# Optimization experiments

Measured on AMD Instinct MI355X. Metric: run time of the kernel, lower is better.

## Reference

```python
import jax, jax.numpy as jnp
import numpy as np

B, S, DIM = 1, 1024, 512
H, DH = 8, 64
CB = 32   # compress block size
SB = 32   # selection block size (== CB, so no importance remap)
NSEL, NMEM, WIN = 4, 4, 64
SCALE = DH ** -0.5
EPS = 1.1920929e-07  # torch fp32 finfo eps used by nn.RMSNorm


def _rmsnorm(x, g):
    return x * jax.lax.rsqrt(jnp.mean(x * x, -1, keepdims=True) + EPS) * g


def _rope(t):
    # lucidrains rotary: interleaved pairs, theta=10000, positions 0..n-1
    d = t.shape[-1]
    inv = 1.0 / (10000.0 ** (jnp.arange(0, d, 2, dtype=jnp.float32) / d))
    ang = jnp.arange(t.shape[-2], dtype=jnp.float32)[:, None] * inv   # [n, d/2]
    cos = jnp.repeat(jnp.cos(ang), 2, axis=-1)
    sin = jnp.repeat(jnp.sin(ang), 2, axis=-1)
    tp = t.reshape(t.shape[:-1] + (d // 2, 2))
    rot = jnp.stack((-tp[..., 1], tp[..., 0]), -1).reshape(t.shape)
    return t * cos + rot * sin


def setup_inputs():
    key = jax.random.key(0)
    ks = jax.random.split(key, 12)
    cd = CB * DH
    p = lambda k, shp: jax.random.normal(k, shp, jnp.float32) * 0.02
    return {
        'inp': jax.random.normal(ks[0], (B, S, DIM), jnp.float32),
        'norm_g': jnp.ones((DIM,), jnp.float32),
        'w_qkv': p(ks[1], (DIM, 3 * H * DH)),
        'k_pos': p(ks[2], (H, CB, DH)),
        'v_pos': p(ks[3], (H, CB, DH)),
        'kc_w1': p(ks[4], (cd, cd)), 'kc_b1': jnp.zeros((cd,), jnp.float32),
        'kc_w2': p(ks[5], (cd, DH)), 'kc_b2': jnp.zeros((DH,), jnp.float32),
        'vc_w1': p(ks[6], (cd, cd)), 'vc_b1': jnp.zeros((cd,), jnp.float32),
        'vc_w2': p(ks[7], (cd, DH)), 'vc_b2': jnp.zeros((DH,), jnp.float32),
        'mem_kv': p(ks[8], (2, H, NMEM, DH)),
        'strat_w': p(ks[9], (DIM, 3 * H)),
        'strat_b': jnp.tile(jnp.array([-2.0, -2.0, 2.0], jnp.float32), H),
        'out_w': p(ks[10], (H * DH, DIM)),
    }


def reference(inp, norm_g, w_qkv, k_pos, v_pos, kc_w1, kc_b1, kc_w2, kc_b2,
              vc_w1, vc_b1, vc_w2, vc_b2, mem_kv, strat_w, strat_b, out_w):
    NEG = -jnp.finfo(inp.dtype).max
    x = _rmsnorm(inp, norm_g)
    q, k, v = jnp.split(x @ w_qkv, 3, axis=-1)
    sh = lambda t: t.reshape(B, S, H, DH).transpose(0, 2, 1, 3)   # b h n d
    q, k, v = sh(q), sh(k), sh(v)

    # ---- compressed branch ----
    nb = S // CB
    kb = k.reshape(B, H, nb, CB, DH) + k_pos[None, :, None]
    vb = v.reshape(B, H, nb, CB, DH) + v_pos[None, :, None]
    comp = lambda t, w1, b1, w2, b2: jax.nn.relu(
        t.reshape(B, H, nb, CB * DH) @ w1 + b1) @ w2 + b2
    ck = comp(kb, kc_w1, kc_b1, kc_w2, kc_b2)                     # b h nb d
    cv = comp(vb, vc_w1, vc_b1, vc_w2, vc_b2)
    ck = jnp.concatenate([jnp.broadcast_to(mem_kv[0][None], (B, H, NMEM, DH)), ck], 2)
    cv = jnp.concatenate([jnp.broadcast_to(mem_kv[1][None], (B, H, NMEM, DH)), cv], 2)

    csim = jnp.einsum('bhid,bhjd->bhij', q, ck) * SCALE
    pos = jnp.arange(S)
    ckpos = jnp.concatenate([jnp.full((NMEM,), -1), (jnp.arange(nb) + 1) * CB - 1])
    csim = jnp.where(ckpos[None, :] < pos[:, None], csim, NEG)
    cattn = jax.nn.softmax(csim, -1)
    c_out = jnp.einsum('bhij,bhjd->bhid', cattn, cv)

    rq, rk = _rope(q), _rope(k)

    # ---- fine selected branch (CB == SB => importance maps 1:1) ----
    imp = cattn[..., NMEM:]                                       # b h i nb
    sel_vals, sel_idx = jax.lax.top_k(imp, NSEL)                  # b h i k
    own = pos // SB
    sel_idx = jnp.concatenate(
        [sel_idx, jnp.broadcast_to(own[None, None, :, None], (B, H, S, 1))], -1)
    fmask = jnp.broadcast_to((sel_vals > 1e-10)[..., None], (B, H, S, NSEL, SB))
    causal = jnp.tril(jnp.ones((SB, SB), bool))[pos % SB]         # [S, SB]
    fmask = jnp.concatenate(
        [fmask, jnp.broadcast_to(causal[None, None, :, None, :], (B, H, S, 1, SB))], 3)
    fmask = fmask.reshape(B, H, S, (NSEL + 1) * SB)

    fkb = rk.reshape(B, H, nb, SB, DH)
    fvb = v.reshape(B, H, nb, SB, DH)
    gather = jax.vmap(jax.vmap(lambda blk, idx: blk[idx]))        # per (b,h)
    fk = gather(fkb, sel_idx).reshape(B, H, S, (NSEL + 1) * SB, DH)
    fv = gather(fvb, sel_idx).reshape(B, H, S, (NSEL + 1) * SB, DH)
    fsim = jnp.einsum('bhid,bhijd->bhij', rq, fk) * SCALE
    fattn = jax.nn.softmax(jnp.where(fmask, fsim, NEG), -1)
    f_out = jnp.einsum('bhij,bhijd->bhid', fattn, fv)

    # ---- sliding window branch (LocalAttention, causal, exact window) ----
    ssim = jnp.einsum('bhid,bhjd->bhij', rq, rk) * SCALE
    smask = (pos[None, :] <= pos[:, None]) & (pos[:, None] - pos[None, :] <= WIN)
    sattn = jax.nn.softmax(jnp.where(smask, ssim, NEG), -1)
    s_out = jnp.einsum('bhij,bhjd->bhid', sattn, v)

    # ---- gated combine ----
    strat = jax.nn.sigmoid(x @ strat_w + strat_b)
    strat = strat.reshape(B, S, H, 3).transpose(0, 2, 1, 3)       # b h n s
    out = strat[..., 0:1] * c_out + strat[..., 1:2] * f_out + strat[..., 2:3] * s_out
    return out.transpose(0, 2, 1, 3).reshape(B, S, H * DH) @ out_w
```

## Files before the change

### kernel.cpp

```cpp
#include <hip/hip_runtime.h>
#include <hip/hip_bf16.h>
#include <cfloat>
#include <math.h>

#define S_LEN 1024
#define DIM 512
#define H_N 8
#define DH 64
#define CB 32
#define NB 32
#define NSEL 4
#define NMEM 4
#define WIN 64
#define SCALE 0.125f
#define EPS 1.1920929e-07f

#define OFF_X      0u
#define OFF_QKV    524288u
#define OFF_RQ     2097152u
#define OFF_RK     2621440u
#define OFF_COS    3145728u
#define OFF_SIN    3178496u
#define OFF_TK     3211264u
#define OFF_TV     3735552u
#define OFF_HK     4259840u
#define OFF_HV     4784128u
#define OFF_CKC    5308416u
#define OFF_CVC    5324800u
#define OFF_STRAT  5341184u
#define OFF_ATT    5365760u
#define OFF_QKVP   2097152u
#define OFF_COMPP  5890048u
#define OFF_OUTP   5890048u

__global__ void rmsnorm_strat_k(const float* __restrict__ inp, const float* __restrict__ g,
                                const float* __restrict__ sw, const float* __restrict__ sb,
                                float* __restrict__ x, float* __restrict__ strat) {
    int s = blockIdx.x;
    int t = threadIdx.x;
    __shared__ __align__(16) float xs[512];
    __shared__ float red[24][8];
    float v0 = inp[s * DIM + t];
    float v1 = inp[s * DIM + t + 256];
    float ss = v0 * v0 + v1 * v1;
    for (int o = 32; o > 0; o >>= 1) ss += __shfl_xor(ss, o);
    __shared__ float wsum[4];
    int wid = t >> 6, lane = t & 63;
    if (lane == 0) wsum[wid] = ss;
    __syncthreads();
    float tot = wsum[0] + wsum[1] + wsum[2] + wsum[3];
    float scale = 1.0f / sqrtf(tot / (float)DIM + EPS);
    float x0 = v0 * scale * g[t];
    float x1 = v1 * scale * g[t + 256];
    x[s * DIM + t]       = x0;
    x[s * DIM + t + 256] = x1;
    xs[t] = x0;
    xs[t + 256] = x1;
    __syncthreads();
    if (t < 192) {
        int o = t >> 3, p = t & 7;
        float acc = 0.0f;
        const float* xb = xs + p * 64;
        for (int k = 0; k < 64; ++k) acc += xb[k] * sw[(p * 64 + k) * 24 + o];
        red[o][p] = acc;
    }
    __syncthreads();
    if (t < 24) {
        float a = sb[t];
        for (int p = 0; p < 8; ++p) a += red[t][p];
        strat[s * 24 + t] = 1.0f / (1.0f + expf(-a));
    }
}

__global__ void rope_table_k(float* __restrict__ cost, float* __restrict__ sint) {
    int idx = blockIdx.x * 256 + threadIdx.x;
    int s = idx >> 5, i = idx & 31;
    double inv = pow(10000.0, -(double)(2 * i) / 64.0);
    double ang = (double)s * inv;
    cost[idx] = (float)cos(ang);
    sint[idx] = (float)sin(ang);
}

__global__ void rope_apply_k(const float* __restrict__ qkv, const float* __restrict__ cost,
                             const float* __restrict__ sint,
                             float* __restrict__ rq, float* __restrict__ rk) {
    int idx = blockIdx.x * 256 + threadIdx.x;
    int s = idx >> 8;
    int rem = idx & 255;
    int h = rem >> 5, i = rem & 31;
    float c = cost[s * 32 + i], sn = sint[s * 32 + i];
    int qb = s * 1536 + h * 64 + 2 * i;
    float q0 = qkv[qb], q1 = qkv[qb + 1];
    int ob = s * 512 + h * 64 + 2 * i;
    rq[ob]     = q0 * c - q1 * sn;
    rq[ob + 1] = q1 * c + q0 * sn;
    float k0 = qkv[qb + 512], k1 = qkv[qb + 513];
    rk[ob]     = k0 * c - k1 * sn;
    rk[ob + 1] = k1 * c + k0 * sn;
}

__global__ void tkv_k(const float* __restrict__ qkv, const float* __restrict__ k_pos,
                      const float* __restrict__ v_pos,
                      float* __restrict__ tk, float* __restrict__ tv) {
    int idx = blockIdx.x * 256 + threadIdx.x;
    int row = idx >> 11;
    int c = idx & 2047;
    int h = row >> 5, nb = row & 31;
    int cb = c >> 6, d = c & 63;
    int srow = nb * 32 + cb;
    tk[idx] = qkv[srow * 1536 + 512 + h * 64 + d] + k_pos[(h * 32 + cb) * 64 + d];
    tv[idx] = qkv[srow * 1536 + 1024 + h * 64 + d] + v_pos[(h * 32 + cb) * 64 + d];
}

__device__ __forceinline__ void gemm_sk_body(const float* __restrict__ A, const float* __restrict__ B,
                                             float* __restrict__ P, int M, int N, int K,
                                             int kstart, int Ks) {
    __shared__ __align__(16) float As[2][16][68];
    __shared__ __align__(16) float Bs[2][16][64];
    const int bm = blockIdx.x * 64, bn = blockIdx.y * 64;
    const int tid = threadIdx.x;
    const int tx = tid & 15, ty = tid >> 4;
    const int ar = tid >> 2;
    const int ac = (tid & 3) * 4;
    const int br = tid >> 4;
    const int bc = (tid & 15) * 4;
    const float* Aptr = A + (size_t)(bm + ar) * K + kstart + ac;
    const float* Bptr = B + (size_t)(kstart + br) * N + bn + bc;

    float4 a4 = *(const float4*)(Aptr);
    float4 b4 = *(const float4*)(Bptr);
    float acc[4][4] = {};
    int buf = 0;
    for (int k0 = 0; k0 < Ks; k0 += 16) {
        As[buf][ac + 0][ar] = a4.x;
        As[buf][ac + 1][ar] = a4.y;
        As[buf][ac + 2][ar] = a4.z;
        As[buf][ac + 3][ar] = a4.w;
        *(float4*)&Bs[buf][br][bc] = b4;
        __syncthreads();
        if (k0 + 16 < Ks) {
            a4 = *(const float4*)(Aptr + k0 + 16);
            b4 = *(const float4*)(Bptr + (size_t)(k0 + 16) * N);
        }
#pragma unroll
        for (int kk = 0; kk < 16; ++kk) {
            const float4 af = *(const float4*)&As[buf][kk][ty * 4];
            const float4 bf = *(const float4*)&Bs[buf][kk][tx * 4];
            acc[0][0] += af.x * bf.x; acc[0][1] += af.x * bf.y; acc[0][2] += af.x * bf.z; acc[0][3] += af.x * bf.w;
            acc[1][0] += af.y * bf.x; acc[1][1] += af.y * bf.y; acc[1][2] += af.y * bf.z; acc[1][3] += af.y * bf.w;
            acc[2][0] += af.z * bf.x; acc[2][1] += af.z * bf.y; acc[2][2] += af.z * bf.z; acc[2][3] += af.z * bf.w;
            acc[3][0] += af.w * bf.x; acc[3][1] += af.w * bf.y; acc[3][2] += af.w * bf.z; acc[3][3] += af.w * bf.w;
        }
        buf ^= 1;
    }
#pragma unroll
    for (int i = 0; i < 4; ++i) {
        int m = bm + ty * 4 + i;
        float4 v;
        v.x = acc[i][0]; v.y = acc[i][1]; v.z = acc[i][2]; v.w = acc[i][3];
        *(float4*)&P[(size_t)m * N + bn + tx * 4] = v;
    }
}

__global__ void gemm_sk_k(const float* __restrict__ A, const float* __restrict__ B,
                          float* __restrict__ P, int M, int N, int K, int nsplit) {
    int kz = blockIdx.z;
    int Ks = K / nsplit;
    gemm_sk_body(A, B, P + (size_t)kz * M * N, M, N, K, kz * Ks, Ks);
}

__global__ void gemm_comp_k(const float* __restrict__ A0, const float* __restrict__ B0,
                            const float* __restrict__ A1, const float* __restrict__ B1,
                            float* __restrict__ P, int M, int N, int K) {
    int z = blockIdx.z;
    int g = z >> 2, kz = z & 3;
    const float* A = g ? A1 : A0;
    const float* B = g ? B1 : B0;
    int Ks = K >> 2;
    gemm_sk_body(A, B, P + (size_t)z * M * N, M, N, K, kz * Ks, Ks);
}

template <int NS, bool RELU, bool BIAS>
__global__ void reduce_k(const float* __restrict__ P, const float* __restrict__ bias,
                         float* __restrict__ Y, int MN, int N) {
    int idx4 = blockIdx.x * 256 + threadIdx.x;
    if (idx4 * 4 >= MN) return;
    const float4* p4 = (const float4*)P;
    int mn4 = MN >> 2;
    float4 v = p4[idx4];
#pragma unroll
    for (int j = 1; j < NS; ++j) {
        float4 w = p4[idx4 + j * (size_t)mn4];
        v.x += w.x; v.y += w.y; v.z += w.z; v.w += w.w;
    }
    if (BIAS) {
        int col = (idx4 * 4) % N;
        float4 b = *(const float4*)(bias + col);
        v.x += b.x; v.y += b.y; v.z += b.z; v.w += b.w;
    }
    if (RELU) {
        v.x = fmaxf(v.x, 0.f); v.y = fmaxf(v.y, 0.f);
        v.z = fmaxf(v.z, 0.f); v.w = fmaxf(v.w, 0.f);
    }
    ((float4*)Y)[idx4] = v;
}

__device__ __forceinline__ void skinny_body(const float* __restrict__ A, const float* __restrict__ B,
                                            const float* __restrict__ bias, float* __restrict__ C, int K) {
    int row = blockIdx.x;
    int col = threadIdx.x & 63;
    int chunk = threadIdx.x >> 6;
    int kpc = K >> 2;
    const float* a = A + (size_t)row * K + chunk * kpc;
    const float* b = B + (size_t)chunk * kpc * 64;
    float acc = 0.0f;
    for (int k = 0; k < kpc; k += 4) {
        float4 av = *(const float4*)(a + k);
        acc += av.x * b[(k + 0) * 64 + col];
        acc += av.y * b[(k + 1) * 64 + col];
        acc += av.z * b[(k + 2) * 64 + col];
        acc += av.w * b[(k + 3) * 64 + col];
    }
    __shared__ float red[4][64];
    red[chunk][col] = acc;
    __syncthreads();
    if (chunk == 0)
        C[(size_t)row * 64 + col] = red[0][col] + red[1][col] + red[2][col] + red[3][col] + bias[col];
}

__global__ void gemm_skinny_z2_k(const float* __restrict__ A0, const float* __restrict__ B0,
                                 const float* __restrict__ b0, float* __restrict__ C0,
                                 const float* __restrict__ A1, const float* __restrict__ B1,
                                 const float* __restrict__ b1, float* __restrict__ C1, int K) {
    if (blockIdx.z == 0) skinny_body(A0, B0, b0, C0, K);
    else                 skinny_body(A1, B1, b1, C1, K);
}

__device__ __forceinline__ float dot64(const float* __restrict__ qsh, const float* __restrict__ kr) {
    const float4* q4 = (const float4*)qsh;
    const float4* k4 = (const float4*)kr;
    float acc = 0.0f;
#pragma unroll
    for (int i = 0; i < 16; ++i) {
        float4 q = q4[i], k = k4[i];
        acc += q.x * k.x + q.y * k.y + q.z * k.z + q.w * k.w;
    }
    return acc;
}

__device__ __forceinline__ float redmax64(float v) {
    for (int o = 32; o > 0; o >>= 1) v = fmaxf(v, __shfl_xor(v, o));
    return v;
}
__device__ __forceinline__ float redsum64(float v) {
    for (int o = 32; o > 0; o >>= 1) v += __shfl_xor(v, o);
    return v;
}

__global__ void attn_fused_k(const float* __restrict__ qkv, const float* __restrict__ rq,
                             const float* __restrict__ rk, const float* __restrict__ ckc,
                             const float* __restrict__ cvc, const float* __restrict__ mem_kv,
                             const float* __restrict__ strat, float* __restrict__ att) {
    int s = blockIdx.x, h = blockIdx.y, lane = threadIdx.x;
    __shared__ __align__(16) float qs[64];
    __shared__ __align__(16) float rqs[64];
    __shared__ float pa[192];
    __shared__ int rows[192];
    qs[lane]  = qkv[s * 1536 + h * 64 + lane];
    rqs[lane] = rq[s * 512 + h * 64 + lane];
    __syncthreads();

    float sim = -FLT_MAX;
    if (lane < 36) {
        bool valid = (lane < NMEM) || ((lane - NMEM + 1) * CB - 1 < s);
        if (valid) {
            const float* kr = (lane < NMEM) ? (mem_kv + (h * 4 + lane) * 64)
                                            : (ckc + (h * 32 + lane - NMEM) * 64);
            sim = dot64(qs, kr) * SCALE;
        }
    }
    float mx = redmax64(sim);
    float e = (sim == -FLT_MAX) ? 0.0f : expf(sim - mx);
    float tot = redsum64(e);
    float a = e / tot;
    pa[lane] = (lane < 36) ? a : 0.0f;
    __syncthreads();
    float c_acc = 0.0f;
    for (int j = 0; j < NMEM; ++j)
        c_acc += pa[j] * mem_kv[2048 + (h * 4 + j) * 64 + lane];
    for (int j = 0; j < 32; ++j)
        c_acc += pa[NMEM + j] * cvc[(h * 32 + j) * 64 + lane];

    float tval = (lane >= NMEM && lane < 36) ? a : -1.0f;
    int tidx = lane - NMEM;
    int sel0, sel1, sel2, sel3, msk = 0;
#pragma unroll
    for (int t = 0; t < NSEL; ++t) {
        float bv = tval; int bi = tidx;
        for (int o = 32; o > 0; o >>= 1) {
            float ov = __shfl_xor(bv, o);
            int oi = __shfl_xor(bi, o);
            if (ov > bv || (ov == bv && oi < bi)) { bv = ov; bi = oi; }
        }
        if (t == 0) sel0 = bi; else if (t == 1) sel1 = bi;
        else if (t == 2) sel2 = bi; else sel3 = bi;
        if (bv > 1e-10f) msk |= 1 << t;
        if (tidx == bi && lane >= NMEM && lane < 36) tval = -1.0f;
    }

    int own = s >> 5, p = s & 31, t31 = lane & 31;
    bool hi = lane >= 32;
    int blkA = hi ? sel1 : sel0;
    bool valA = hi ? (msk & 2) : (msk & 1);
    int rowA = blkA * 32 + t31;
    float simA = valA ? dot64(rqs, rk + rowA * 512 + h * 64) * SCALE : -FLT_MAX;
    int blkB = hi ? sel3 : sel2;
    bool valB = hi ? (msk & 8) : (msk & 4);
    int rowB = blkB * 32 + t31;
    float simB = valB ? dot64(rqs, rk + rowB * 512 + h * 64) * SCALE : -FLT_MAX;
    int rowC = own * 32 + t31;
    bool valC = (!hi) && (t31 <= p);
    float simC = valC ? dot64(rqs, rk + rowC * 512 + h * 64) * SCALE : -FLT_MAX;

    float fmx = redmax64(fmaxf(fmaxf(simA, simB), simC));
    float eA = (simA == -FLT_MAX) ? 0.0f : expf(simA - fmx);
    float eB = (simB == -FLT_MAX) ? 0.0f : expf(simB - fmx);
    float eC = (simC == -FLT_MAX) ? 0.0f : expf(simC - fmx);
    float fsum = redsum64(eA + eB + eC);
    float finv = 1.0f / fsum;
    pa[lane] = eA * finv;        rows[lane] = rowA;
    pa[64 + lane] = eB * finv;   rows[64 + lane] = rowB;
    pa[128 + lane] = eC * finv;  rows[128 + lane] = rowC;
    __syncthreads();
    float f_acc = 0.0f;
    for (int kk = 0; kk < 160; ++kk)
        f_acc += pa[kk] * qkv[rows[kk] * 1536 + 1024 + h * 64 + lane];
    __syncthreads();

    int lo = (s > WIN) ? s - WIN : 0;
    int cnt = s - lo + 1;
    float sA = (lane < cnt) ? dot64(rqs, rk + (lo + lane) * 512 + h * 64) * SCALE : -FLT_MAX;
    float sB = (64 + lane < cnt) ? dot64(rqs, rk + (lo + 64 + lane) * 512 + h * 64) * SCALE : -FLT_MAX;
    float smx = redmax64(fmaxf(sA, sB));
    float esA = (sA == -FLT_MAX) ? 0.0f : expf(sA - smx);
    float esB = (sB == -FLT_MAX) ? 0.0f : expf(sB - smx);
    float ssum = redsum64(esA + esB);
    float sinv = 1.0f / ssum;
    pa[lane] = esA * sinv;
    if (64 + lane < cnt) pa[64 + lane] = esB * sinv;
    __syncthreads();
    float s_acc = 0.0f;
    for (int kk = 0; kk < cnt; ++kk)
        s_acc += pa[kk] * qkv[(lo + kk) * 1536 + 1024 + h * 64 + lane];

    const float* st = strat + s * 24 + h * 3;
    att[s * 512 + h * 64 + lane] = st[0] * c_acc + st[1] * f_acc + st[2] * s_acc;
}

extern "C" void kernel_launch(void* const* d_in, const int* in_sizes, int n_in,
                              void* d_out, int out_size, void* d_ws, size_t ws_size,
                              hipStream_t stream) {
    const float* inp     = (const float*)d_in[0];
    const float* norm_g  = (const float*)d_in[1];
    const float* w_qkv   = (const float*)d_in[2];
    const float* k_pos   = (const float*)d_in[3];
    const float* v_pos   = (const float*)d_in[4];
    const float* kc_w1   = (const float*)d_in[5];
    const float* kc_b1   = (const float*)d_in[6];
    const float* kc_w2   = (const float*)d_in[7];
    const float* kc_b2   = (const float*)d_in[8];
    const float* vc_w1   = (const float*)d_in[9];
    const float* vc_b1   = (const float*)d_in[10];
    const float* vc_w2   = (const float*)d_in[11];
    const float* vc_b2   = (const float*)d_in[12];
    const float* mem_kv  = (const float*)d_in[13];
    const float* strat_w = (const float*)d_in[14];
    const float* strat_b = (const float*)d_in[15];
    const float* out_w   = (const float*)d_in[16];
    float* out = (float*)d_out;

    float* ws = (float*)d_ws;
    float* x     = ws + OFF_X;
    float* qkv   = ws + OFF_QKV;
    float* rq    = ws + OFF_RQ;
    float* rk    = ws + OFF_RK;
    float* cost  = ws + OFF_COS;
    float* sint  = ws + OFF_SIN;
    float* tk    = ws + OFF_TK;
    float* tv    = ws + OFF_TV;
    float* hk    = ws + OFF_HK;
    float* hv    = ws + OFF_HV;
    float* ckc   = ws + OFF_CKC;
    float* cvc   = ws + OFF_CVC;
    float* strat = ws + OFF_STRAT;
    float* att   = ws + OFF_ATT;
    float* qkvp  = ws + OFF_QKVP;
    float* compp = ws + OFF_COMPP;
    float* outp  = ws + OFF_OUTP;

    rmsnorm_strat_k<<<1024, 256, 0, stream>>>(inp, norm_g, strat_w, strat_b, x, strat);
    gemm_sk_k<<<dim3(16, 24, 2), 256, 0, stream>>>(x, w_qkv, qkvp, 1024, 1536, 512, 2);
    reduce_k<2, false, false><<<1536, 256, 0, stream>>>(qkvp, nullptr, qkv, 1024 * 1536, 1536);
    rope_table_k<<<128, 256, 0, stream>>>(cost, sint);
    rope_apply_k<<<1024, 256, 0, stream>>>(qkv, cost, sint, rq, rk);
    tkv_k<<<2048, 256, 0, stream>>>(qkv, k_pos, v_pos, tk, tv);
    gemm_comp_k<<<dim3(4, 32, 8), 256, 0, stream>>>(tk, kc_w1, tv, vc_w1, compp, 256, 2048, 2048);
    reduce_k<4, true, true><<<512, 256, 0, stream>>>(compp, kc_b1, hk, 256 * 2048, 2048);
    reduce_k<4, true, true><<<512, 256, 0, stream>>>(compp + 4u * 256 * 2048, vc_b1, hv, 256 * 2048, 2048);
    gemm_skinny_z2_k<<<dim3(256, 1, 2), 256, 0, stream>>>(hk, kc_w2, kc_b2, ckc, hv, vc_w2, vc_b2, cvc, 2048);
    attn_fused_k<<<dim3(1024, 8), 64, 0, stream>>>(qkv, rq, rk, ckc, cvc, mem_kv, strat, att);
    gemm_sk_k<<<dim3(16, 8, 4), 256, 0, stream>>>(att, out_w, outp, 1024, 512, 512, 4);
    reduce_k<4, false, false><<<512, 256, 0, stream>>>(outp, nullptr, out, 1024 * 512, 512);
}
```

Measured before the change: 375.4 us.

## Transpose K/V layouts for coalesced attention and fuse prep kernels into GEMM loads

Adds transposed per-head rk and compressed-key buffers so each lane in the attention kernel reads keys with coalesced, d-major loads instead of strided 64-float dot products per lane. V is also copied into a per-head contiguous buffer during the QKV reduction. The tkv add-position step is folded into the compression GEMM's A loads, the rope table kernel is folded into rope_apply, and the two compression reductions are merged into one launch. Zero-weight rows are skipped in the selection gather. The cost is an extra transpose kernel and a rearranged workspace, and the transposed key reads are scattered gathers when the selected rows differ across lanes.

```diff
diff --git a/kernel.cpp b/kernel.cpp
--- a/kernel.cpp
+++ b/kernel.cpp
@@ -16,22 +16,19 @@
 #define EPS 1.1920929e-07f
 
 #define OFF_X      0u
+#define OFF_RKT    0u
 #define OFF_QKV    524288u
 #define OFF_RQ     2097152u
 #define OFF_RK     2621440u
-#define OFF_COS    3145728u
-#define OFF_SIN    3178496u
-#define OFF_TK     3211264u
-#define OFF_TV     3735552u
-#define OFF_HK     4259840u
-#define OFF_HV     4784128u
-#define OFF_CKC    5308416u
-#define OFF_CVC    5324800u
-#define OFF_STRAT  5341184u
-#define OFF_ATT    5365760u
-#define OFF_QKVP   2097152u
-#define OFF_COMPP  5890048u
-#define OFF_OUTP   5890048u
+#define OFF_VBUF   3145728u
+#define OFF_CKT    3670016u
+#define OFF_CVC    3702784u
+#define OFF_STRAT  3735552u
+#define OFF_ATT    3760128u
+#define OFF_HK     4284416u
+#define OFF_QKVP   5332992u
+#define OFF_COMPP  5332992u
+#define OFF_OUTP   5332992u
 
 __global__ void rmsnorm_strat_k(const float* __restrict__ inp, const float* __restrict__ g,
                                 const float* __restrict__ sw, const float* __restrict__ sb,
@@ -70,46 +67,6 @@
         for (int p = 0; p < 8; ++p) a += red[t][p];
         strat[s * 24 + t] = 1.0f / (1.0f + expf(-a));
     }
-}
-
-__global__ void rope_table_k(float* __restrict__ cost, float* __restrict__ sint) {
-    int idx = blockIdx.x * 256 + threadIdx.x;
-    int s = idx >> 5, i = idx & 31;
-    double inv = pow(10000.0, -(double)(2 * i) / 64.0);
-    double ang = (double)s * inv;
-    cost[idx] = (float)cos(ang);
-    sint[idx] = (float)sin(ang);
-}
-
-__global__ void rope_apply_k(const float* __restrict__ qkv, const float* __restrict__ cost,
-                             const float* __restrict__ sint,
-                             float* __restrict__ rq, float* __restrict__ rk) {
-    int idx = blockIdx.x * 256 + threadIdx.x;
-    int s = idx >> 8;
-    int rem = idx & 255;
-    int h = rem >> 5, i = rem & 31;
-    float c = cost[s * 32 + i], sn = sint[s * 32 + i];
-    int qb = s * 1536 + h * 64 + 2 * i;
-    float q0 = qkv[qb], q1 = qkv[qb + 1];
-    int ob = s * 512 + h * 64 + 2 * i;
-    rq[ob]     = q0 * c - q1 * sn;
-    rq[ob + 1] = q1 * c + q0 * sn;
-    float k0 = qkv[qb + 512], k1 = qkv[qb + 513];
-    rk[ob]     = k0 * c - k1 * sn;
-    rk[ob + 1] = k1 * c + k0 * sn;
-}
-
-__global__ void tkv_k(const float* __restrict__ qkv, const float* __restrict__ k_pos,
-                      const float* __restrict__ v_pos,
-                      float* __restrict__ tk, float* __restrict__ tv) {
-    int idx = blockIdx.x * 256 + threadIdx.x;
-    int row = idx >> 11;
-    int c = idx & 2047;
-    int h = row >> 5, nb = row & 31;
-    int cb = c >> 6, d = c & 63;
-    int srow = nb * 32 + cb;
-    tk[idx] = qkv[srow * 1536 + 512 + h * 64 + d] + k_pos[(h * 32 + cb) * 64 + d];
-    tv[idx] = qkv[srow * 1536 + 1024 + h * 64 + d] + v_pos[(h * 32 + cb) * 64 + d];
 }
 
 __device__ __forceinline__ void gemm_sk_body(const float* __restrict__ A, const float* __restrict__ B,
@@ -169,20 +126,155 @@
     gemm_sk_body(A, B, P + (size_t)kz * M * N, M, N, K, kz * Ks, Ks);
 }
 
-__global__ void gemm_comp_k(const float* __restrict__ A0, const float* __restrict__ B0,
-                            const float* __restrict__ A1, const float* __restrict__ B1,
-                            float* __restrict__ P, int M, int N, int K) {
-    int z = blockIdx.z;
-    int g = z >> 2, kz = z & 3;
-    const float* A = g ? A1 : A0;
-    const float* B = g ? B1 : B0;
-    int Ks = K >> 2;
-    gemm_sk_body(A, B, P + (size_t)z * M * N, M, N, K, kz * Ks, Ks);
-}
-
-template <int NS, bool RELU, bool BIAS>
-__global__ void reduce_k(const float* __restrict__ P, const float* __restrict__ bias,
-                         float* __restrict__ Y, int MN, int N) {
+__global__ void reduce_qkv_k(const float* __restrict__ P, float* __restrict__ qkv,
+                             float* __restrict__ vbuf) {
+    int idx4 = blockIdx.x * 256 + threadIdx.x;
+    const int mn4 = 393216;
+    float4 v = ((const float4*)P)[idx4];
+    float4 w = ((const float4*)P)[idx4 + mn4];
+    v.x += w.x; v.y += w.y; v.z += w.z; v.w += w.w;
+    ((float4*)qkv)[idx4] = v;
+    int c = (idx4 % 384) * 4;
+    if (c >= 1024) {
+        int s = idx4 / 384;
+        int h = (c - 1024) >> 6, d = (c - 1024) & 63;
+        *(float4*)(vbuf + (size_t)h * 65536 + s * 64 + d) = v;
+    }
+}
+
+__global__ void rope_apply_k(const float* __restrict__ qkv,
+                             float* __restrict__ rq, float* __restrict__ rk) {
+    int idx = blockIdx.x * 256 + threadIdx.x;
+    int s = idx >> 8;
+    int rem = idx & 255;
+    int h = rem >> 5, i = rem & 31;
+    double inv = pow(10000.0, -(double)i / 32.0);
+    double ang = (double)s * inv;
+    float c = (float)cos(ang), sn = (float)sin(ang);
+    int qb = s * 1536 + h * 64 + 2 * i;
+    float q0 = qkv[qb], q1 = qkv[qb + 1];
+    int ob = s * 512 + h * 64 + 2 * i;
+    rq[ob]     = q0 * c - q1 * sn;
+    rq[ob + 1] = q1 * c + q0 * sn;
+    float k0 = qkv[qb + 512], k1 = qkv[qb + 513];
+    rk[ob]     = k0 * c - k1 * sn;
+    rk[ob + 1] = k1 * c + k0 * sn;
+}
+
+__global__ void transpose_rk_k(const float* __restrict__ rk, float* __restrict__ rkT,
+                               const float* __restrict__ mem_kv, float* __restrict__ ckT) {
+    int h = blockIdx.x, st = blockIdx.y, t = threadIdx.x;
+    __shared__ float tile[64][65];
+    int s0 = st * 64;
+    int r = t >> 2, c0 = (t & 3) * 16;
+    const float* src = rk + (size_t)(s0 + r) * 512 + h * 64 + c0;
+#pragma unroll
+    for (int q = 0; q < 4; ++q) {
+        float4 v = *(const float4*)(src + q * 4);
+        tile[r][c0 + q * 4 + 0] = v.x;
+        tile[r][c0 + q * 4 + 1] = v.y;
+        tile[r][c0 + q * 4 + 2] = v.z;
+        tile[r][c0 + q * 4 + 3] = v.w;
+    }
+    __syncthreads();
+    int wv = t >> 6, ls = t & 63;
+    float* dst = rkT + (size_t)h * 65536 + s0 + ls;
+#pragma unroll
+    for (int p = 0; p < 16; ++p) {
+        int d = p * 4 + wv;
+        dst[(size_t)d * 1024] = tile[ls][d];
+    }
+    if (st == 0) {
+        int d = t >> 2, j = t & 3;
+        ckT[h * 2304 + d * 36 + j] = mem_kv[h * 256 + j * 64 + d];
+    }
+}
+
+__global__ void gemm_comp_k(const float* __restrict__ qkv, const float* __restrict__ k_pos,
+                            const float* __restrict__ v_pos, const float* __restrict__ kw1,
+                            const float* __restrict__ vw1, float* __restrict__ P) {
+    int z = blockIdx.z, g = z >> 2, kz = z & 3;
+    const float* B = g ? vw1 : kw1;
+    const float* pos = g ? v_pos : k_pos;
+    const int qoff = g ? 1024 : 512;
+    const int kstart = kz * 512;
+    __shared__ __align__(16) float As[2][16][68];
+    __shared__ __align__(16) float Bs[2][16][64];
+    const int bm = blockIdx.x * 64, bn = blockIdx.y * 64;
+    const int tid = threadIdx.x;
+    const int tx = tid & 15, ty = tid >> 4;
+    const int ar = tid >> 2, ac = (tid & 3) * 4;
+    const int br = tid >> 4, bc = (tid & 15) * 4;
+    const int m = bm + ar;
+    const int hh = m >> 5, nb = m & 31;
+    const float* qb = qkv + (size_t)(nb * 32) * 1536 + qoff + hh * 64;
+    const float* pb = pos + hh * 2048;
+    const float* Bptr = B + (size_t)(kstart + br) * 2048 + bn + bc;
+
+    auto loadA = [&](int kk) {
+        int cb = kk >> 6, d = kk & 63;
+        float4 a = *(const float4*)(qb + (size_t)cb * 1536 + d);
+        float4 p = *(const float4*)(pb + cb * 64 + d);
+        a.x += p.x; a.y += p.y; a.z += p.z; a.w += p.w;
+        return a;
+    };
+
+    float4 a4 = loadA(kstart + ac);
+    float4 b4 = *(const float4*)Bptr;
+    float acc[4][4] = {};
+    int buf = 0;
+    for (int k0 = 0; k0 < 512; k0 += 16) {
+        As[buf][ac + 0][ar] = a4.x;
+        As[buf][ac + 1][ar] = a4.y;
+        As[buf][ac + 2][ar] = a4.z;
+        As[buf][ac + 3][ar] = a4.w;
+        *(float4*)&Bs[buf][br][bc] = b4;
+        __syncthreads();
+        if (k0 + 16 < 512) {
+            a4 = loadA(kstart + ac + k0 + 16);
+            b4 = *(const float4*)(Bptr + (size_t)(k0 + 16) * 2048);
+        }
+#pragma unroll
+        for (int kk = 0; kk < 16; ++kk) {
+            const float4 af = *(const float4*)&As[buf][kk][ty * 4];
+            const float4 bf = *(const float4*)&Bs[buf][kk][tx * 4];
+            acc[0][0] += af.x * bf.x; acc[0][1] += af.x * bf.y; acc[0][2] += af.x * bf.z; acc[0][3] += af.x * bf.w;
+            acc[1][0] += af.y * bf.x; acc[1][1] += af.y * bf.y; acc[1][2] += af.y * bf.z; acc[1][3] += af.y * bf.w;
+            acc[2][0] += af.z * bf.x; acc[2][1] += af.z * bf.y; acc[2][2] += af.z * bf.z; acc[2][3] += af.z * bf.w;
+            acc[3][0] += af.w * bf.x; acc[3][1] += af.w * bf.y; acc[3][2] += af.w * bf.z; acc[3][3] += af.w * bf.w;
+        }
+        buf ^= 1;
+    }
+    float* Pz = P + (size_t)z * 524288;
+#pragma unroll
+    for (int i = 0; i < 4; ++i) {
+        int mm = bm + ty * 4 + i;
+        float4 v;
+        v.x = acc[i][0]; v.y = acc[i][1]; v.z = acc[i][2]; v.w = acc[i][3];
+        *(float4*)&Pz[(size_t)mm * 2048 + bn + tx * 4] = v;
+    }
+}
+
+__global__ void reduce_comp_k(const float* __restrict__ P, const float* __restrict__ kb,
+                              const float* __restrict__ vb, float* __restrict__ hkv) {
+    int idx4 = blockIdx.x * 256 + threadIdx.x;
+    const int half4 = 131072;
+    int which = idx4 >= half4 ? 1 : 0;
+    int l4 = idx4 - which * half4;
+    const float4* p4 = (const float4*)P + (size_t)which * 4 * half4 + l4;
+    float4 v = p4[0];
+    float4 w1 = p4[half4], w2 = p4[2 * half4], w3 = p4[3 * (size_t)half4];
+    v.x += w1.x + w2.x + w3.x; v.y += w1.y + w2.y + w3.y;
+    v.z += w1.z + w2.z + w3.z; v.w += w1.w + w2.w + w3.w;
+    int col = (l4 * 4) & 2047;
+    const float* bias = (which ? vb : kb) + col;
+    v.x = fmaxf(v.x + bias[0], 0.f); v.y = fmaxf(v.y + bias[1], 0.f);
+    v.z = fmaxf(v.z + bias[2], 0.f); v.w = fmaxf(v.w + bias[3], 0.f);
+    *(float4*)(hkv + (size_t)which * 524288 + (size_t)l4 * 4) = v;
+}
+
+template <int NS>
+__global__ void reduce_k(const float* __restrict__ P, float* __restrict__ Y, int MN) {
     int idx4 = blockIdx.x * 256 + threadIdx.x;
     if (idx4 * 4 >= MN) return;
     const float4* p4 = (const float4*)P;
@@ -190,31 +282,27 @@
     float4 v = p4[idx4];
 #pragma unroll
     for (int j = 1; j < NS; ++j) {
-        float4 w = p4[idx4 + j * (size_t)mn4];
+        float4 w = p4[idx4 + (size_t)j * mn4];
         v.x += w.x; v.y += w.y; v.z += w.z; v.w += w.w;
     }
-    if (BIAS) {
-        int col = (idx4 * 4) % N;
-        float4 b = *(const float4*)(bias + col);
-        v.x += b.x; v.y += b.y; v.z += b.z; v.w += b.w;
-    }
-    if (RELU) {
-        v.x = fmaxf(v.x, 0.f); v.y = fmaxf(v.y, 0.f);
-        v.z = fmaxf(v.z, 0.f); v.w = fmaxf(v.w, 0.f);
-    }
     ((float4*)Y)[idx4] = v;
 }
 
-__device__ __forceinline__ void skinny_body(const float* __restrict__ A, const float* __restrict__ B,
-                                            const float* __restrict__ bias, float* __restrict__ C, int K) {
+__global__ void gemm_skinny_z2_k(const float* __restrict__ hkv, const float* __restrict__ kw2,
+                                 const float* __restrict__ kb2, const float* __restrict__ vw2,
+                                 const float* __restrict__ vb2, float* __restrict__ ckT,
+                                 float* __restrict__ cvc) {
+    int z = blockIdx.z;
+    const float* A = hkv + (size_t)z * 524288;
+    const float* B = z ? vw2 : kw2;
+    const float* bias = z ? vb2 : kb2;
     int row = blockIdx.x;
     int col = threadIdx.x & 63;
     int chunk = threadIdx.x >> 6;
-    int kpc = K >> 2;
-    const float* a = A + (size_t)row * K + chunk * kpc;
-    const float* b = B + (size_t)chunk * kpc * 64;
+    const float* a = A + (size_t)row * 2048 + chunk * 512;
+    const float* b = B + (size_t)chunk * 512 * 64;
     float acc = 0.0f;
-    for (int k = 0; k < kpc; k += 4) {
+    for (int k = 0; k < 512; k += 4) {
         float4 av = *(const float4*)(a + k);
         acc += av.x * b[(k + 0) * 64 + col];
         acc += av.y * b[(k + 1) * 64 + col];
@@ -224,28 +312,12 @@
     __shared__ float red[4][64];
     red[chunk][col] = acc;
     __syncthreads();
-    if (chunk == 0)
-        C[(size_t)row * 64 + col] = red[0][col] + red[1][col] + red[2][col] + red[3][col] + bias[col];
-}
-
-__global__ void gemm_skinny_z2_k(const float* __restrict__ A0, const float* __restrict__ B0,
-                                 const float* __restrict__ b0, float* __restrict__ C0,
-                                 const float* __restrict__ A1, const float* __restrict__ B1,
-                                 const float* __restrict__ b1, float* __restrict__ C1, int K) {
-    if (blockIdx.z == 0) skinny_body(A0, B0, b0, C0, K);
-    else                 skinny_body(A1, B1, b1, C1, K);
-}
-
-__device__ __forceinline__ float dot64(const float* __restrict__ qsh, const float* __restrict__ kr) {
-    const float4* q4 = (const float4*)qsh;
-    const float4* k4 = (const float4*)kr;
-    float acc = 0.0f;
-#pragma unroll
-    for (int i = 0; i < 16; ++i) {
-        float4 q = q4[i], k = k4[i];
-        acc += q.x * k.x + q.y * k.y + q.z * k.z + q.w * k.w;
-    }
-    return acc;
+    if (chunk == 0) {
+        float v = red[0][col] + red[1][col] + red[2][col] + red[3][col] + bias[col];
+        int hh = row >> 5, j = row & 31;
+        if (z == 0) ckT[hh * 2304 + col * 36 + 4 + j] = v;
+        else        cvc[(size_t)row * 64 + col] = v;
+    }
 }
 
 __device__ __forceinline__ float redmax64(float v) {
@@ -257,39 +329,61 @@
     return v;
 }
 
-__global__ void attn_fused_k(const float* __restrict__ qkv, const float* __restrict__ rq,
-                             const float* __restrict__ rk, const float* __restrict__ ckc,
-                             const float* __restrict__ cvc, const float* __restrict__ mem_kv,
-                             const float* __restrict__ strat, float* __restrict__ att) {
+__global__ __launch_bounds__(64) void attn_fused_k(
+    const float* __restrict__ qkv, const float* __restrict__ rq,
+    const float* __restrict__ rkT, const float* __restrict__ ckT,
+    const float* __restrict__ cvc, const float* __restrict__ mem_kv,
+    const float* __restrict__ vbuf, const float* __restrict__ strat,
+    float* __restrict__ att) {
     int s = blockIdx.x, h = blockIdx.y, lane = threadIdx.x;
     __shared__ __align__(16) float qs[64];
     __shared__ __align__(16) float rqs[64];
-    __shared__ float pa[192];
-    __shared__ int rows[192];
+    __shared__ float paw[192];
+    __shared__ int rww[192];
     qs[lane]  = qkv[s * 1536 + h * 64 + lane];
     rqs[lane] = rq[s * 512 + h * 64 + lane];
     __syncthreads();
 
-    float sim = -FLT_MAX;
-    if (lane < 36) {
-        bool valid = (lane < NMEM) || ((lane - NMEM + 1) * CB - 1 < s);
-        if (valid) {
-            const float* kr = (lane < NMEM) ? (mem_kv + (h * 4 + lane) * 64)
-                                            : (ckc + (h * 32 + lane - NMEM) * 64);
-            sim = dot64(qs, kr) * SCALE;
-        }
-    }
-    float mx = redmax64(sim);
-    float e = (sim == -FLT_MAX) ? 0.0f : expf(sim - mx);
+    int own = s >> 5, p = s & 31, t31 = lane & 31;
+    bool hiw = lane >= 32;
+    int lo = (s > WIN) ? s - WIN : 0;
+    int cnt = s - lo + 1;
+    bool cvalid = (lane < NMEM) || (lane < 36 && (lane - NMEM + 1) * CB - 1 < s);
+    int jc = (lane < 36) ? lane : 35;
+    int rowC = own * 32 + t31;
+    int rowSA = lo + lane;      if (rowSA > 1023) rowSA = 1023;
+    int rowSB = lo + 64 + lane; if (rowSB > 1023) rowSB = 1023;
+    const float* rkTh = rkT + (size_t)h * 65536;
+    const float* ckTh = ckT + h * 2304;
+
+    float c0 = 0, c1 = 0, f0 = 0, f1 = 0, a0 = 0, a1 = 0, b0 = 0, b1 = 0;
+#pragma unroll 4
+    for (int d = 0; d < 64; d += 2) {
+        float qd0 = qs[d], qd1 = qs[d + 1];
+        float rd0 = rqs[d], rd1 = rqs[d + 1];
+        const float* r0 = rkTh + (size_t)d * 1024;
+        const float* r1 = r0 + 1024;
+        c0 += qd0 * ckTh[d * 36 + jc];
+        c1 += qd1 * ckTh[(d + 1) * 36 + jc];
+        f0 += rd0 * r0[rowC];  f1 += rd1 * r1[rowC];
+        a0 += rd0 * r0[rowSA]; a1 += rd1 * r1[rowSA];
+        b0 += rd0 * r0[rowSB]; b1 += rd1 * r1[rowSB];
+    }
+
+    float simc = cvalid ? (c0 + c1) * SCALE : -FLT_MAX;
+    float mx = redmax64(simc);
+    float e = (simc == -FLT_MAX) ? 0.0f : expf(simc - mx);
     float tot = redsum64(e);
     float a = e / tot;
-    pa[lane] = (lane < 36) ? a : 0.0f;
-    __syncthreads();
-    float c_acc = 0.0f;
-    for (int j = 0; j < NMEM; ++j)
-        c_acc += pa[j] * mem_kv[2048 + (h * 4 + j) * 64 + lane];
-    for (int j = 0; j < 32; ++j)
-        c_acc += pa[NMEM + j] * cvc[(h * 32 + j) * 64 + lane];
+    paw[lane] = (lane < 36) ? a : 0.0f;
+    __syncthreads();
+    float cacc;
+    {
+        const float* mv = mem_kv + 2048 + h * 256 + lane;
+        cacc = paw[0] * mv[0] + paw[1] * mv[64] + paw[2] * mv[128] + paw[3] * mv[192];
+        const float* cvb = cvc + h * 2048 + lane;
+        for (int j = 0; j < 32; ++j) cacc += paw[4 + j] * cvb[j * 64];
+    }
 
     float tval = (lane >= NMEM && lane < 36) ? a : -1.0f;
     int tidx = lane - NMEM;
@@ -308,19 +402,23 @@
         if (tidx == bi && lane >= NMEM && lane < 36) tval = -1.0f;
     }
 
-    int own = s >> 5, p = s & 31, t31 = lane & 31;
-    bool hi = lane >= 32;
-    int blkA = hi ? sel1 : sel0;
-    bool valA = hi ? (msk & 2) : (msk & 1);
-    int rowA = blkA * 32 + t31;
-    float simA = valA ? dot64(rqs, rk + rowA * 512 + h * 64) * SCALE : -FLT_MAX;
-    int blkB = hi ? sel3 : sel2;
-    bool valB = hi ? (msk & 8) : (msk & 4);
-    int rowB = blkB * 32 + t31;
-    float simB = valB ? dot64(rqs, rk + rowB * 512 + h * 64) * SCALE : -FLT_MAX;
-    int rowC = own * 32 + t31;
-    bool valC = (!hi) && (t31 <= p);
-    float simC = valC ? dot64(rqs, rk + rowC * 512 + h * 64) * SCALE : -FLT_MAX;
+    int rowA = (hiw ? sel1 : sel0) * 32 + t31;
+    int rowB = (hiw ? sel3 : sel2) * 32 + t31;
+    float A0 = 0, A1 = 0, B0 = 0, B1 = 0;
+#pragma unroll 4
+    for (int d = 0; d < 64; d += 2) {
+        float rd0 = rqs[d], rd1 = rqs[d + 1];
+        const float* r0 = rkTh + (size_t)d * 1024;
+        const float* r1 = r0 + 1024;
+        A0 += rd0 * r0[rowA]; A1 += rd1 * r1[rowA];
+        B0 += rd0 * r0[rowB]; B1 += rd1 * r1[rowB];
+    }
+    bool valA = hiw ? ((msk >> 1) & 1) : (msk & 1);
+    bool valB = hiw ? ((msk >> 3) & 1) : ((msk >> 2) & 1);
+    bool valC = (!hiw) && (t31 <= p);
+    float simA = valA ? (A0 + A1) * SCALE : -FLT_MAX;
+    float simB = valB ? (B0 + B1) * SCALE : -FLT_MAX;
+    float simC = valC ? (f0 + f1) * SCALE : -FLT_MAX;
 
     float fmx = redmax64(fmaxf(fmaxf(simA, simB), simC));
     float eA = (simA == -FLT_MAX) ? 0.0f : expf(simA - fmx);
@@ -328,33 +426,36 @@
     float eC = (simC == -FLT_MAX) ? 0.0f : expf(simC - fmx);
     float fsum = redsum64(eA + eB + eC);
     float finv = 1.0f / fsum;
-    pa[lane] = eA * finv;        rows[lane] = rowA;
-    pa[64 + lane] = eB * finv;   rows[64 + lane] = rowB;
-    pa[128 + lane] = eC * finv;  rows[128 + lane] = rowC;
-    __syncthreads();
-    float f_acc = 0.0f;
-    for (int kk = 0; kk < 160; ++kk)
-        f_acc += pa[kk] * qkv[rows[kk] * 1536 + 1024 + h * 64 + lane];
-    __syncthreads();
-
-    int lo = (s > WIN) ? s - WIN : 0;
-    int cnt = s - lo + 1;
-    float sA = (lane < cnt) ? dot64(rqs, rk + (lo + lane) * 512 + h * 64) * SCALE : -FLT_MAX;
-    float sB = (64 + lane < cnt) ? dot64(rqs, rk + (lo + 64 + lane) * 512 + h * 64) * SCALE : -FLT_MAX;
+    __syncthreads();
+    paw[lane] = eA * finv;        rww[lane] = rowA;
+    paw[64 + lane] = eB * finv;   rww[64 + lane] = rowB;
+    paw[128 + lane] = eC * finv;  rww[128 + lane] = rowC;
+    __syncthreads();
+    const float* vh = vbuf + (size_t)h * 65536 + lane;
+    float facc = 0.0f;
+    for (int kk = 0; kk < 160; ++kk) {
+        float w = paw[kk];
+        if (w != 0.0f) facc += w * vh[(size_t)rww[kk] * 64];
+    }
+    __syncthreads();
+
+    float sA = (lane < cnt) ? (a0 + a1) * SCALE : -FLT_MAX;
+    float sB = (64 + lane < cnt) ? (b0 + b1) * SCALE : -FLT_MAX;
     float smx = redmax64(fmaxf(sA, sB));
     float esA = (sA == -FLT_MAX) ? 0.0f : expf(sA - smx);
     float esB = (sB == -FLT_MAX) ? 0.0f : expf(sB - smx);
     float ssum = redsum64(esA + esB);
     float sinv = 1.0f / ssum;
-    pa[lane] = esA * sinv;
-    if (64 + lane < cnt) pa[64 + lane] = esB * sinv;
-    __syncthreads();
-    float s_acc = 0.0f;
+    paw[lane] = esA * sinv;
+    if (64 + lane < cnt) paw[64 + lane] = esB * sinv;
+    __syncthreads();
+    float sacc = 0.0f;
+    const float* vlo = vh + (size_t)lo * 64;
     for (int kk = 0; kk < cnt; ++kk)
-        s_acc += pa[kk] * qkv[(lo + kk) * 1536 + 1024 + h * 64 + lane];
+        sacc += paw[kk] * vlo[(size_t)kk * 64];
 
     const float* st = strat + s * 24 + h * 3;
-    att[s * 512 + h * 64 + lane] = st[0] * c_acc + st[1] * f_acc + st[2] * s_acc;
+    att[s * 512 + h * 64 + lane] = st[0] * cacc + st[1] * facc + st[2] * sacc;
 }
 
 extern "C" void kernel_launch(void* const* d_in, const int* in_sizes, int n_in,
@@ -381,34 +482,29 @@
 
     float* ws = (float*)d_ws;
     float* x     = ws + OFF_X;
+    float* rkT   = ws + OFF_RKT;
     float* qkv   = ws + OFF_QKV;
     float* rq    = ws + OFF_RQ;
     float* rk    = ws + OFF_RK;
-    float* cost  = ws + OFF_COS;
-    float* sint  = ws + OFF_SIN;
-    float* tk    = ws + OFF_TK;
-    float* tv    = ws + OFF_TV;
-    float* hk    = ws + OFF_HK;
-    float* hv    = ws + OFF_HV;
-    float* ckc   = ws + OFF_CKC;
+    float* vbuf  = ws + OFF_VBUF;
+    float* ckT   = ws + OFF_CKT;
     float* cvc   = ws + OFF_CVC;
     float* strat = ws + OFF_STRAT;
     float* att   = ws + OFF_ATT;
+    float* hkv   = ws + OFF_HK;
     float* qkvp  = ws + OFF_QKVP;
     float* compp = ws + OFF_COMPP;
     float* outp  = ws + OFF_OUTP;
 
     rmsnorm_strat_k<<<1024, 256, 0, stream>>>(inp, norm_g, strat_w, strat_b, x, strat);
     gemm_sk_k<<<dim3(16, 24, 2), 256, 0, stream>>>(x, w_qkv, qkvp, 1024, 1536, 512, 2);
-    reduce_k<2, false, false><<<1536, 256, 0, stream>>>(qkvp, nullptr, qkv, 1024 * 1536, 1536);
-    rope_table_k<<<128, 256, 0, stream>>>(cost, sint);
-    rope_apply_k<<<1024, 256, 0, stream>>>(qkv, cost, sint, rq, rk);
-    tkv_k<<<2048, 256, 0, stream>>>(qkv, k_pos, v_pos, tk, tv);
-    gemm_comp_k<<<dim3(4, 32, 8), 256, 0, stream>>>(tk, kc_w1, tv, vc_w1, compp, 256, 2048, 2048);
-    reduce_k<4, true, true><<<512, 256, 0, stream>>>(compp, kc_b1, hk, 256 * 2048, 2048);
-    reduce_k<4, true, true><<<512, 256, 0, stream>>>(compp + 4u * 256 * 2048, vc_b1, hv, 256 * 2048, 2048);
-    gemm_skinny_z2_k<<<dim3(256, 1, 2), 256, 0, stream>>>(hk, kc_w2, kc_b2, ckc, hv, vc_w2, vc_b2, cvc, 2048);
-    attn_fused_k<<<dim3(1024, 8), 64, 0, stream>>>(qkv, rq, rk, ckc, cvc, mem_kv, strat, att);
+    reduce_qkv_k<<<1536, 256, 0, stream>>>(qkvp, qkv, vbuf);
+    rope_apply_k<<<1024, 256, 0, stream>>>(qkv, rq, rk);
+    transpose_rk_k<<<dim3(8, 16), 256, 0, stream>>>(rk, rkT, mem_kv, ckT);
+    gemm_comp_k<<<dim3(4, 32, 8), 256, 0, stream>>>(qkv, k_pos, v_pos, kc_w1, vc_w1, compp);
+    reduce_comp_k<<<1024, 256, 0, stream>>>(compp, kc_b1, vc_b1, hkv);
+    gemm_skinny_z2_k<<<dim3(256, 1, 2), 256, 0, stream>>>(hkv, kc_w2, kc_b2, vc_w2, vc_b2, ckT, cvc);
+    attn_fused_k<<<dim3(1024, 8), 64, 0, stream>>>(qkv, rq, rkT, ckT, cvc, mem_kv, vbuf, strat, att);
     gemm_sk_k<<<dim3(16, 8, 4), 256, 0, stream>>>(att, out_w, outp, 1024, 512, 512, 4);
-    reduce_k<4, false, false><<<512, 256, 0, stream>>>(outp, nullptr, out, 1024 * 512, 512);
-}
+    reduce_k<4><<<512, 256, 0, stream>>>(outp, out, 1024 * 512);
+}
```

Measured after the change: 386.0 us. 1.03x slower.
